# Kernel tuning notes

Hardware: AMD Instinct MI355X
Metric: run time of the kernel (lower is better)

## Reference

```python
import jax, jax.numpy as jnp
import numpy as np


def setup_inputs() -> dict:
    key = jax.random.key(0)
    k1, k2 = jax.random.split(key)
    N, L, C = 64, 256, 384
    x = jax.random.normal(k1, (N, L, C), dtype=jnp.float32)
    # frame counts per phoneme, 1..16
    durations = jax.random.randint(k2, (N, L), 1, 17, dtype=jnp.int32)
    # expand_max_len = max over batch of total duration (static Python int)
    mel_max_length = int(jnp.max(jnp.sum(durations, axis=-1)))
    return {"x": x, "durations": durations, "mel_max_length": mel_max_length}


def reference(x, durations, mel_max_length):
    # Equivalent to: alignment[n, t, j] = 1 if starts[n,j] <= t < csum[n,j];
    # output = alignment @ x. Implemented as a direct gather via cumulative
    # durations (searchsorted), avoiding the O(N*T*L) one-hot matmul.
    N, L, C = x.shape
    csum = jnp.cumsum(durations, axis=-1)            # [N, L] exclusive end per phoneme
    t = jnp.arange(mel_max_length)                   # [T]
    # source phoneme index for each output frame: first j with t < csum[j]
    idx = jax.vmap(lambda c: jnp.searchsorted(c, t, side='right'))(csum)  # [N, T]
    total = csum[:, -1]                              # [N] total frames per example
    valid = t[None, :] < total[:, None]              # [N, T]
    idx = jnp.minimum(idx, L - 1)
    out = jnp.take_along_axis(x, idx[..., None], axis=1)   # [N, T, C]
    out = jnp.where(valid[..., None], out, jnp.zeros((), dtype=x.dtype))
    mel_pos = jnp.arange(1, mel_max_length + 1, dtype=jnp.int64)[None, :]  # [1, T]
    return out, mel_pos
```

## Files before the change

kernel.cpp:

```cpp
#include <hip/hip_runtime.h>

#define N_B   64
#define L_IN  256
#define C_DIM 384
#define C4    (C_DIM / 4)

__global__ __launch_bounds__(256) void lr_idx_kernel(const int* __restrict__ dur,
                                                     int* __restrict__ idx_out,
                                                     float* __restrict__ melpos,
                                                     int melmax) {
    __shared__ int csum[L_IN];
    const int n = blockIdx.x;
    const int tid = threadIdx.x;

    csum[tid] = dur[n * L_IN + tid];
    __syncthreads();
    #pragma unroll
    for (int off = 1; off < L_IN; off <<= 1) {
        int add = (tid >= off) ? csum[tid - off] : 0;
        __syncthreads();
        csum[tid] += add;
        __syncthreads();
    }
    const int total = csum[L_IN - 1];

    for (int t = tid; t < melmax; t += 256) {
        int r = -1;
        if (t < total) {
            int lo = 0, hi = L_IN;
            #pragma unroll
            for (int s = 0; s < 8; ++s) {
                int mid = (lo + hi) >> 1;
                if (csum[mid] <= t) lo = mid + 1; else hi = mid;
            }
            r = (lo < (L_IN - 1)) ? lo : (L_IN - 1);
        }
        idx_out[n * melmax + t] = r;
        if (n == 0) melpos[t] = (float)(t + 1);
    }
}

__global__ __launch_bounds__(256) void lr_gather_kernel(const float4* __restrict__ x,
                                                        const int* __restrict__ idx,
                                                        float4* __restrict__ out,
                                                        int melmax) {
    const int n     = blockIdx.x & 63;
    const int chunk = blockIdx.x >> 6;
    const int off   = chunk * 256 + (int)threadIdx.x;
    const int row_f4 = melmax * C4;
    if (off >= row_f4) return;

    const int t  = off / C4;
    const int c4 = off - t * C4;

    const int r = idx[n * melmax + t];
    float4 v = make_float4(0.f, 0.f, 0.f, 0.f);
    if (r >= 0) v = x[(n * L_IN + r) * C4 + c4];
    out[(size_t)n * row_f4 + off] = v;
}

extern "C" void kernel_launch(void* const* d_in, const int* in_sizes, int n_in,
                              void* d_out, int out_size, void* d_ws, size_t ws_size,
                              hipStream_t stream) {
    const float* x  = (const float*)d_in[0];
    const int* dur  = (const int*)d_in[1];
    const int melmax = out_size / (N_B * C_DIM + 1);

    int* idxbuf = (int*)d_ws;
    float* mp   = (float*)d_out + (size_t)N_B * melmax * C_DIM;

    lr_idx_kernel<<<N_B, 256, 0, stream>>>(dur, idxbuf, mp, melmax);

    const int chunks_per_n = (melmax * C4 + 255) / 256;
    lr_gather_kernel<<<chunks_per_n * N_B, 256, 0, stream>>>(
        (const float4*)x, idxbuf, (float4*)d_out, melmax);
}
```

Before: 276.3 us.

## Fuse index search into gather kernel with per-block scan and nontemporal stores

Merges the separate index-computation kernel into the gather kernel. Each block now redoes the 256-element prefix scan over durations and binary-searches only the ~22 frames it covers, keeping the row indices in shared memory. Each block also handles 2048 float4s instead of 256, and output writes use nontemporal stores. This removes the global index buffer and the dependency between two launches, at the cost of repeating the scan in every block. Mel positions move to a small separate kernel.

```diff
diff --git a/kernel.cpp b/kernel.cpp
--- a/kernel.cpp
+++ b/kernel.cpp
@@ -1,17 +1,27 @@
 #include <hip/hip_runtime.h>
 
-#define N_B   64
-#define L_IN  256
-#define C_DIM 384
-#define C4    (C_DIM / 4)
+#define N_B    64
+#define L_IN   256
+#define C_DIM  384
+#define C4     (C_DIM / 4)
+#define F4_PER_BLOCK 2048
 
-__global__ __launch_bounds__(256) void lr_idx_kernel(const int* __restrict__ dur,
-                                                     int* __restrict__ idx_out,
-                                                     float* __restrict__ melpos,
-                                                     int melmax) {
+typedef float vfloat4 __attribute__((ext_vector_type(4)));
+
+__global__ __launch_bounds__(256) void lr_fused_kernel(const vfloat4* __restrict__ x,
+                                                       const int* __restrict__ dur,
+                                                       vfloat4* __restrict__ out,
+                                                       int melmax) {
     __shared__ int csum[L_IN];
-    const int n = blockIdx.x;
-    const int tid = threadIdx.x;
+    __shared__ int r_tab[32];
+
+    const int n      = blockIdx.x & 63;
+    const int bchunk = blockIdx.x >> 6;
+    const int tid    = (int)threadIdx.x;
+    const int row_f4 = melmax * C4;
+    const int start  = bchunk * F4_PER_BLOCK;
+    if (start >= row_f4) return;
+    const int end    = min(start + F4_PER_BLOCK, row_f4);
 
     csum[tid] = dur[n * L_IN + tid];
     __syncthreads();
@@ -24,7 +34,11 @@
     }
     const int total = csum[L_IN - 1];
 
-    for (int t = tid; t < melmax; t += 256) {
+    const int t0    = start / C4;
+    const int tlast = (end - 1) / C4;
+    const int tcnt  = tlast - t0 + 1;
+    if (tid < tcnt) {
+        const int t = t0 + tid;
         int r = -1;
         if (t < total) {
             int lo = 0, hi = L_IN;
@@ -35,28 +49,24 @@
             }
             r = (lo < (L_IN - 1)) ? lo : (L_IN - 1);
         }
-        idx_out[n * melmax + t] = r;
-        if (n == 0) melpos[t] = (float)(t + 1);
+        r_tab[tid] = r;
+    }
+    __syncthreads();
+
+    const size_t obase = (size_t)n * row_f4;
+    for (int off = start + tid; off < end; off += 256) {
+        const int t  = off / C4;
+        const int c4 = off - t * C4;
+        const int r  = r_tab[t - t0];
+        vfloat4 v = (vfloat4)0.f;
+        if (r >= 0) v = x[(n * L_IN + r) * C4 + c4];
+        __builtin_nontemporal_store(v, &out[obase + off]);
     }
 }
 
-__global__ __launch_bounds__(256) void lr_gather_kernel(const float4* __restrict__ x,
-                                                        const int* __restrict__ idx,
-                                                        float4* __restrict__ out,
-                                                        int melmax) {
-    const int n     = blockIdx.x & 63;
-    const int chunk = blockIdx.x >> 6;
-    const int off   = chunk * 256 + (int)threadIdx.x;
-    const int row_f4 = melmax * C4;
-    if (off >= row_f4) return;
-
-    const int t  = off / C4;
-    const int c4 = off - t * C4;
-
-    const int r = idx[n * melmax + t];
-    float4 v = make_float4(0.f, 0.f, 0.f, 0.f);
-    if (r >= 0) v = x[(n * L_IN + r) * C4 + c4];
-    out[(size_t)n * row_f4 + off] = v;
+__global__ __launch_bounds__(256) void lr_melpos_kernel(float* __restrict__ mp, int melmax) {
+    int t = blockIdx.x * 256 + threadIdx.x;
+    if (t < melmax) mp[t] = (float)(t + 1);
 }
 
 extern "C" void kernel_launch(void* const* d_in, const int* in_sizes, int n_in,
@@ -66,12 +76,12 @@
     const int* dur  = (const int*)d_in[1];
     const int melmax = out_size / (N_B * C_DIM + 1);
 
-    int* idxbuf = (int*)d_ws;
-    float* mp   = (float*)d_out + (size_t)N_B * melmax * C_DIM;
+    const int row_f4 = melmax * C4;
+    const int blocks_per_n = (row_f4 + F4_PER_BLOCK - 1) / F4_PER_BLOCK;
 
-    lr_idx_kernel<<<N_B, 256, 0, stream>>>(dur, idxbuf, mp, melmax);
+    lr_fused_kernel<<<blocks_per_n * N_B, 256, 0, stream>>>(
+        (const vfloat4*)x, dur, (vfloat4*)d_out, melmax);
 
-    const int chunks_per_n = (melmax * C4 + 255) / 256;
-    lr_gather_kernel<<<chunks_per_n * N_B, 256, 0, stream>>>(
-        (const float4*)x, idxbuf, (float4*)d_out, melmax);
+    float* mp = (float*)d_out + (size_t)N_B * melmax * C_DIM;
+    lr_melpos_kernel<<<(melmax + 255) / 256, 256, 0, stream>>>(mp, melmax);
 }
```

Result: faster. 268.0 us (-3.0%).
